# Kernel tuning notes

Measured on AMD Instinct MI355X. Metric: run time of the kernel, lower is better.

The kernel has to match this reference:

```python
import jax, jax.numpy as jnp
import numpy as np

FEAT_STRIDE = 16
SCALES = (8.0, 16.0, 32.0)
RATIOS = (0.5, 1.0, 2.0)
NEG_TH = 0.3
POS_TH = 0.7
FG_FRACTION = 0.5
RPN_BATCHSIZE = 256
A = 9  # num anchors per location


def generate_anchors(base_size=16, ratios=RATIOS, scales=SCALES):
    """Standard py-faster-rcnn anchor generation (ratio-major, scale-minor)."""
    base = np.array([0.0, 0.0, base_size - 1.0, base_size - 1.0])
    w = base[2] - base[0] + 1.0
    h = base[3] - base[1] + 1.0
    xc = base[0] + 0.5 * (w - 1.0)
    yc = base[1] + 0.5 * (h - 1.0)
    ratios = np.asarray(ratios, dtype=np.float64)
    scales = np.asarray(scales, dtype=np.float64)
    size = w * h
    ws = np.round(np.sqrt(size / ratios))          # [3]
    hs = np.round(ws * ratios)                     # [3]
    ws = (ws[:, None] * scales[None, :]).reshape(-1)  # [9]
    hs = (hs[:, None] * scales[None, :]).reshape(-1)
    anchors = np.stack([xc - 0.5 * (ws - 1.0), yc - 0.5 * (hs - 1.0),
                        xc + 0.5 * (ws - 1.0), yc + 0.5 * (hs - 1.0)], axis=1)
    return anchors.astype(np.float32)  # [9,4]


def _rank_desc(scores, mask):
    """Rank (0 = largest) of each element among masked entries, per row."""
    s = jnp.where(mask, scores, -jnp.inf)
    order = jnp.argsort(-s, axis=1)
    return jnp.argsort(order, axis=1)


def setup_inputs() -> dict:
    key = jax.random.key(0)
    k1, k2, k3, k4, k5, k6 = jax.random.split(key, 6)
    B, K, H, W = 32, 50, 64, 64
    IMG = float(H * FEAT_STRIDE)  # 1024
    rpn_cls_score = jax.random.normal(k1, (B, 2 * A, H, W), dtype=jnp.float32)
    x1 = jax.random.uniform(k2, (B, K)) * (IMG - 220.0)
    y1 = jax.random.uniform(k3, (B, K)) * (IMG - 220.0)
    bw = jax.random.uniform(k4, (B, K)) * 180.0 + 16.0
    bh = jax.random.uniform(k5, (B, K)) * 180.0 + 16.0
    gt_boxes = jnp.stack([x1, y1, x1 + bw, y1 + bh, jnp.ones((B, K))], axis=-1).astype(jnp.float32)
    im_info = jnp.tile(jnp.array([[IMG, IMG, 1.0]], dtype=jnp.float32), (B, 1))
    num_boxes = jax.random.randint(k6, (B,), 1, K + 1).astype(jnp.int32)
    return {"rpn_cls_score": rpn_cls_score, "gt_boxes": gt_boxes,
            "im_info": im_info, "num_boxes": num_boxes}


def reference(rpn_cls_score, gt_boxes, im_info, num_boxes):
    B = gt_boxes.shape[0]
    K = gt_boxes.shape[1]
    H, W = rpn_cls_score.shape[2], rpn_cls_score.shape[3]

    anchors = jnp.asarray(generate_anchors())  # [A,4]
    sx = jnp.arange(W, dtype=jnp.float32) * FEAT_STRIDE
    sy = jnp.arange(H, dtype=jnp.float32) * FEAT_STRIDE
    gx, gy = jnp.meshgrid(sx, sy)  # [H,W]
    shifts = jnp.stack([gx.ravel(), gy.ravel(), gx.ravel(), gy.ravel()], axis=1)  # [HW,4]
    all_anchors = (anchors[None, :, :] + shifts[:, None, :]).reshape(-1, 4)  # [N,4], N=HW*A
    N = all_anchors.shape[0]

    im_h, im_w = im_info[0, 0], im_info[0, 1]
    inside = ((all_anchors[:, 0] >= 0) & (all_anchors[:, 1] >= 0) &
              (all_anchors[:, 2] < im_w) & (all_anchors[:, 3] < im_h))  # [N]

    # pairwise IoU [B,N,K] with +1 pixel convention
    gt4 = gt_boxes[..., :4]
    ax1, ay1, ax2, ay2 = (all_anchors[None, :, None, i] for i in range(4))
    gx1, gy1, gx2, gy2 = (gt4[:, None, :, i] for i in range(4))
    iw = jnp.maximum(jnp.minimum(ax2, gx2) - jnp.maximum(ax1, gx1) + 1.0, 0.0)
    ih = jnp.maximum(jnp.minimum(ay2, gy2) - jnp.maximum(ay1, gy1) + 1.0, 0.0)
    inter = iw * ih
    a_area = ((all_anchors[:, 2] - all_anchors[:, 0] + 1.0) *
              (all_anchors[:, 3] - all_anchors[:, 1] + 1.0))[None, :, None]
    g_area = ((gt4[..., 2] - gt4[..., 0] + 1.0) * (gt4[..., 3] - gt4[..., 1] + 1.0))[:, None, :]
    ov = inter / (a_area + g_area - inter)
    valid = (jnp.arange(K)[None, :] < num_boxes[:, None])  # [B,K]
    ov = jnp.where(valid[:, None, :], ov, -1.0)

    max_ov = ov.max(axis=2)       # [B,N]
    argmax = ov.argmax(axis=2)    # [B,N]
    gt_max = ov.max(axis=1)       # [B,K]
    gt_max = jnp.where(gt_max == 0.0, 1e-5, gt_max)
    best = ((ov == gt_max[:, None, :]) & valid[:, None, :]).any(axis=2)  # [B,N]

    lab = jnp.full((B, N), -1.0, dtype=jnp.float32)
    lab = jnp.where(inside[None, :] & (max_ov < NEG_TH), 0.0, lab)
    lab = jnp.where(inside[None, :] & best, 1.0, lab)
    lab = jnp.where(inside[None, :] & (max_ov >= POS_TH), 1.0, lab)

    # random subsampling of positives / negatives
    skey = jax.random.key(42)
    kf, kb = jax.random.split(skey)
    num_fg = int(FG_FRACTION * RPN_BATCHSIZE)
    fg_mask = lab == 1.0
    rk_fg = _rank_desc(jax.random.uniform(kf, (B, N)), fg_mask)
    lab = jnp.where(fg_mask & (rk_fg >= num_fg), -1.0, lab)
    fg_cnt = (lab == 1.0).sum(axis=1)
    num_bg = RPN_BATCHSIZE - fg_cnt  # [B]
    bg_mask = lab == 0.0
    rk_bg = _rank_desc(jax.random.uniform(kb, (B, N)), bg_mask)
    lab = jnp.where(bg_mask & (rk_bg >= num_bg[:, None]), -1.0, lab)

    assigned = jnp.take_along_axis(gt4, argmax[:, :, None], axis=1)  # [B,N,4]
    ew = all_anchors[:, 2] - all_anchors[:, 0] + 1.0
    eh = all_anchors[:, 3] - all_anchors[:, 1] + 1.0
    ecx = all_anchors[:, 0] + 0.5 * ew
    ecy = all_anchors[:, 1] + 0.5 * eh
    gw = assigned[..., 2] - assigned[..., 0] + 1.0
    gh = assigned[..., 3] - assigned[..., 1] + 1.0
    gcx = assigned[..., 0] + 0.5 * gw
    gcy = assigned[..., 1] + 0.5 * gh
    tgt = jnp.stack([(gcx - ecx[None]) / ew[None], (gcy - ecy[None]) / eh[None],
                     jnp.log(gw / ew[None]), jnp.log(gh / eh[None])], axis=-1)  # [B,N,4]
    tgt = jnp.where(inside[None, :, None], tgt, 0.0)

    in_w = jnp.where((lab == 1.0)[:, :, None], 1.0, 0.0) * jnp.ones((4,), jnp.float32)
    num_examples = (lab >= 0.0).sum(axis=1).astype(jnp.float32)  # [B]
    out_w = jnp.where((lab >= 0.0)[:, :, None], (1.0 / num_examples)[:, None, None], 0.0) \
            * jnp.ones((4,), jnp.float32)

    labels_out = lab.reshape(B, H, W, A).transpose(0, 3, 1, 2).reshape(B, 1, A * H, W)
    tgt_out = tgt.reshape(B, H, W, A * 4).transpose(0, 3, 1, 2)
    in_w_out = in_w.reshape(B, H, W, A * 4).transpose(0, 3, 1, 2)
    out_w_out = out_w.reshape(B, H, W, A * 4).transpose(0, 3, 1, 2)
    return (labels_out, tgt_out, in_w_out, out_w_out)
```

## Files before the change

### kernel.cpp

```cpp
#include <hip/hip_runtime.h>
#include <stdint.h>

#pragma clang fp contract(off)

#define NBATCH 32
#define NK 50
#define NH 64
#define NW 64
#define NA 9
#define NN (NH * NW * NA)
#define BN (NBATCH * NN)
#define HWSZ (NH * NW)
#define BLK_PER_B (NN / 256)

constexpr size_t OFF_AMAX  = 0;
constexpr size_t OFF_PK    = OFF_AMAX + (size_t)BN * 4;
constexpr size_t OFF_GTMAX = OFF_PK + (size_t)BN * 4;
constexpr size_t OFF_NUMEX = OFF_GTMAX + (size_t)NBATCH * NK * 4;

constexpr size_t OUT_LAB  = 0;
constexpr size_t OUT_TGT  = (size_t)NBATCH * NA * HWSZ;
constexpr size_t OUT_INW  = OUT_TGT + (size_t)NBATCH * NA * 4 * HWSZ;
constexpr size_t OUT_OUTW = OUT_INW + (size_t)NBATCH * NA * 4 * HWSZ;

__constant__ float c_anch[NA][4] = {
    {-84.f, -40.f, 99.f, 55.f},    {-176.f, -88.f, 191.f, 103.f},
    {-360.f, -184.f, 375.f, 199.f}, {-56.f, -56.f, 71.f, 71.f},
    {-120.f, -120.f, 135.f, 135.f}, {-248.f, -248.f, 263.f, 263.f},
    {-36.f, -80.f, 51.f, 95.f},    {-80.f, -168.f, 95.f, 183.f},
    {-168.f, -344.f, 183.f, 359.f}};

struct TF2 { uint32_t a, b; };

__host__ __device__ constexpr uint32_t rotl32(uint32_t x, int d) {
  return (x << d) | (x >> (32 - d));
}

__host__ __device__ constexpr TF2 threefry2x32(uint32_t k0, uint32_t k1,
                                               uint32_t x0, uint32_t x1) {
  uint32_t ks2 = k0 ^ k1 ^ 0x1BD11BDAu;
  x0 += k0; x1 += k1;
  x0 += x1; x1 = rotl32(x1, 13); x1 ^= x0;
  x0 += x1; x1 = rotl32(x1, 15); x1 ^= x0;
  x0 += x1; x1 = rotl32(x1, 26); x1 ^= x0;
  x0 += x1; x1 = rotl32(x1, 6);  x1 ^= x0;
  x0 += k1; x1 += ks2 + 1u;
  x0 += x1; x1 = rotl32(x1, 17); x1 ^= x0;
  x0 += x1; x1 = rotl32(x1, 29); x1 ^= x0;
  x0 += x1; x1 = rotl32(x1, 16); x1 ^= x0;
  x0 += x1; x1 = rotl32(x1, 24); x1 ^= x0;
  x0 += ks2; x1 += k0 + 2u;
  x0 += x1; x1 = rotl32(x1, 13); x1 ^= x0;
  x0 += x1; x1 = rotl32(x1, 15); x1 ^= x0;
  x0 += x1; x1 = rotl32(x1, 26); x1 ^= x0;
  x0 += x1; x1 = rotl32(x1, 6);  x1 ^= x0;
  x0 += k0; x1 += k1 + 3u;
  x0 += x1; x1 = rotl32(x1, 17); x1 ^= x0;
  x0 += x1; x1 = rotl32(x1, 29); x1 ^= x0;
  x0 += x1; x1 = rotl32(x1, 16); x1 ^= x0;
  x0 += x1; x1 = rotl32(x1, 24); x1 ^= x0;
  x0 += k1; x1 += ks2 + 4u;
  x0 += x1; x1 = rotl32(x1, 13); x1 ^= x0;
  x0 += x1; x1 = rotl32(x1, 15); x1 ^= x0;
  x0 += x1; x1 = rotl32(x1, 26); x1 ^= x0;
  x0 += x1; x1 = rotl32(x1, 6);  x1 ^= x0;
  x0 += ks2; x1 += k0 + 5u;
  return TF2{x0, x1};
}

constexpr TF2 KEY_FG = threefry2x32(0u, 42u, 0u, 0u);
constexpr TF2 KEY_BG = threefry2x32(0u, 42u, 0u, 1u);

__device__ inline uint32_t rand23(uint32_t k0, uint32_t k1, uint32_t idx) {
  TF2 r = threefry2x32(k0, k1, 0u, idx);
  return (r.a ^ r.b) >> 9;
}

__device__ inline void anchor_of(int n, float& x1, float& y1, float& x2, float& y2) {
  int a = n % NA;
  int s = n / NA;
  int xx = s % NW;
  int yy = s / NW;
  float sx = (float)(xx * 16);
  float sy = (float)(yy * 16);
  x1 = c_anch[a][0] + sx; y1 = c_anch[a][1] + sy;
  x2 = c_anch[a][2] + sx; y2 = c_anch[a][3] + sy;
}

__device__ inline float iou1(float ax1, float ay1, float ax2, float ay2,
                             float gx1, float gy1, float gx2, float gy2) {
  float iw = fminf(ax2, gx2) - fmaxf(ax1, gx1) + 1.0f;
  iw = fmaxf(iw, 0.0f);
  float ih = fminf(ay2, gy2) - fmaxf(ay1, gy1) + 1.0f;
  ih = fmaxf(ih, 0.0f);
  float inter = iw * ih;
  float aa = (ax2 - ax1 + 1.0f) * (ay2 - ay1 + 1.0f);
  float ga = (gx2 - gx1 + 1.0f) * (gy2 - gy1 + 1.0f);
  return inter / (aa + ga - inter);
}

__global__ __launch_bounds__(256) void k_gtmax(const float* __restrict__ gt,
                                               const int* __restrict__ nbox,
                                               float* __restrict__ gtmax) {
  int b = blockIdx.x / NK;
  int k = blockIdx.x % NK;
  if (k >= nbox[b]) {
    if (threadIdx.x == 0) gtmax[blockIdx.x] = -1.0f;
    return;
  }
  const float* g = gt + ((size_t)b * NK + k) * 5;
  float gx1 = g[0], gy1 = g[1], gx2 = g[2], gy2 = g[3];
  float m = 0.0f;
#pragma unroll
  for (int a = 0; a < NA; ++a) {
    float bx1 = c_anch[a][0], by1 = c_anch[a][1];
    float bx2 = c_anch[a][2], by2 = c_anch[a][3];
    int ix_lo = max(0, (int)floorf((gx1 - 1.0f - bx2) * 0.0625f) - 1);
    int ix_hi = min(NW - 1, (int)ceilf((gx2 + 1.0f - bx1) * 0.0625f) + 1);
    int iy_lo = max(0, (int)floorf((gy1 - 1.0f - by2) * 0.0625f) - 1);
    int iy_hi = min(NH - 1, (int)ceilf((gy2 + 1.0f - by1) * 0.0625f) + 1);
    if (ix_lo > ix_hi || iy_lo > iy_hi) continue;
    int nx = ix_hi - ix_lo + 1;
    int ny = iy_hi - iy_lo + 1;
    int lg = 32 - __clz(nx - 1);
    int tot = ny << lg;
    unsigned mask = (1u << lg) - 1u;
    for (int c = threadIdx.x; c < tot; c += 256) {
      int ixo = c & mask;
      if (ixo >= nx) continue;
      int ix = ix_lo + ixo;
      int iy = iy_lo + (c >> lg);
      float sx = (float)(ix * 16), sy = (float)(iy * 16);
      m = fmaxf(m, iou1(bx1 + sx, by1 + sy, bx2 + sx, by2 + sy, gx1, gy1, gx2, gy2));
    }
  }
  for (int o = 1; o < 64; o <<= 1) m = fmaxf(m, __shfl_xor(m, o));
  __shared__ float ws4[4];
  if ((threadIdx.x & 63) == 0) ws4[threadIdx.x >> 6] = m;
  __syncthreads();
  if (threadIdx.x == 0) {
    m = fmaxf(fmaxf(ws4[0], ws4[1]), fmaxf(ws4[2], ws4[3]));
    if (m == 0.0f) m = 1e-5f;
    gtmax[blockIdx.x] = m;
  }
}

__global__ __launch_bounds__(256) void k_label(const float* __restrict__ gt,
                                               const int* __restrict__ nbox,
                                               const float* __restrict__ gtmax,
                                               const float* __restrict__ iminfo,
                                               unsigned* __restrict__ pkarr,
                                               int* __restrict__ amax) {
  int b = blockIdx.x / BLK_PER_B;
  int n = (blockIdx.x % BLK_PER_B) * 256 + threadIdx.x;
  __shared__ float sg[NK * 5];
  __shared__ float sgm[NK];
  __shared__ float sga[NK];
  if (threadIdx.x < NK * 5) sg[threadIdx.x] = gt[(size_t)b * NK * 5 + threadIdx.x];
  if (threadIdx.x < NK) sgm[threadIdx.x] = gtmax[b * NK + threadIdx.x];
  __syncthreads();
  if (threadIdx.x < NK) {
    float* gg = sg + threadIdx.x * 5;
    sga[threadIdx.x] = (gg[2] - gg[0] + 1.0f) * (gg[3] - gg[1] + 1.0f);
  }
  __syncthreads();

  float ax1, ay1, ax2, ay2;
  anchor_of(n, ax1, ay1, ax2, ay2);
  float aa = (ax2 - ax1 + 1.0f) * (ay2 - ay1 + 1.0f);
  int m = nbox[b];
  float best = -2.0f;
  int bi = 0;
  bool isbest = false;
  for (int k = 0; k < m; ++k) {
    float iw = fminf(ax2, sg[k * 5 + 2]) - fmaxf(ax1, sg[k * 5]) + 1.0f;
    iw = fmaxf(iw, 0.0f);
    float ih = fminf(ay2, sg[k * 5 + 3]) - fmaxf(ay1, sg[k * 5 + 1]) + 1.0f;
    ih = fmaxf(ih, 0.0f);
    float inter = iw * ih;
    float ov = inter / (aa + sga[k] - inter);
    if (ov > best) { best = ov; bi = k; }
    if (ov == sgm[k]) isbest = true;
  }
  float imh = iminfo[0], imw = iminfo[1];
  bool inside = (ax1 >= 0.0f) && (ay1 >= 0.0f) && (ax2 < imw) && (ay2 < imh);
  int lab = -1;
  if (inside) {
    if (best < 0.3f) lab = 0;
    if (isbest) lab = 1;
    if (best >= 0.7f) lab = 1;
  }
  int t = b * NN + n;
  uint32_t kk0 = (lab == 1) ? KEY_FG.a : KEY_BG.a;
  uint32_t kk1 = (lab == 1) ? KEY_FG.b : KEY_BG.b;
  uint32_t v = rand23(kk0, kk1, (uint32_t)t);
  pkarr[t] = (v << 2) | (uint32_t)(lab + 1);
  amax[t] = bi;
}

__global__ __launch_bounds__(1024) void k_select(unsigned* __restrict__ pkarr,
                                                 float* __restrict__ numex) {
  int b = blockIdx.x >> 1;
  int cls = blockIdx.x & 1;
  int base_lab = b * NN;
  unsigned wantcode = (cls == 0) ? 2u : 1u;
  int tid = threadIdx.x;

  __shared__ unsigned h1s[4096];
  __shared__ unsigned listV[2048];
  __shared__ unsigned listI[2048];
  __shared__ unsigned waveTot[4];
  __shared__ int sFG, sBG, sBs, sR1, sCross;
  __shared__ unsigned sCnt;
  for (int i = tid; i < 4096; i += 1024) h1s[i] = 0;
  if (tid == 0) { sFG = 0; sBG = 0; sCross = -1; sCnt = 0; }
  __syncthreads();

  const uint4* pk4 = (const uint4*)(pkarr + base_lab);

  int cfg = 0, cbg = 0;
  for (int i = tid; i < NN / 4; i += 1024) {
    uint4 P4 = pk4[i];
    unsigned pks[4] = {P4.x, P4.y, P4.z, P4.w};
#pragma unroll
    for (int j = 0; j < 4; ++j) {
      unsigned code = pks[j] & 3u;
      cfg += (code == 2u);
      cbg += (code == 1u);
      if (code == wantcode) atomicAdd(&h1s[pks[j] >> 13], 1u);
    }
  }
  for (int o = 1; o < 64; o <<= 1) { cfg += __shfl_xor(cfg, o); cbg += __shfl_xor(cbg, o); }
  if ((tid & 63) == 0) { atomicAdd(&sFG, cfg); atomicAdd(&sBG, cbg); }
  __syncthreads();

  int fg = sFG, bg = sBG;
  int fgk = min(fg, 128);
  int total, C;
  if (cls == 0) {
    total = fg; C = 128;
  } else {
    total = bg; C = 256 - fgk;
    if (tid == 0) numex[b] = (float)(fgk + min(bg, C));
  }
  if (total <= C) return;

  unsigned myChunk = 0, suf = 0;
  if (tid < 256) {
    for (int j = 0; j < 16; ++j) myChunk += h1s[tid * 16 + j];
    unsigned ss = myChunk;
    int lane = tid & 63;
#pragma unroll
    for (int o = 1; o < 64; o <<= 1) {
      unsigned t2 = __shfl_down(ss, o);
      if (lane + o < 64) ss += t2;
    }
    suf = ss;
    if (lane == 0) waveTot[tid >> 6] = ss;
  }
  __syncthreads();
  if (tid < 256) {
    int w = tid >> 6;
    for (int w2 = w + 1; w2 < 4; ++w2) suf += waveTot[w2];
    if (suf >= (unsigned)C) atomicMax(&sCross, tid);
  }
  __syncthreads();
  if (tid == sCross) {
    unsigned cum = suf - myChunk;
    int i = tid * 16 + 15;
    for (;; --i) {
      unsigned c = h1s[i];
      if (cum + c >= (unsigned)C) break;
      cum += c;
    }
    sBs = i; sR1 = (int)((unsigned)C - cum);
  }
  __syncthreads();
  int Bs = sBs;
  unsigned r1 = (unsigned)sR1;

  for (int i = tid; i < NN / 4; i += 1024) {
    uint4 P4 = pk4[i];
    unsigned pks[4] = {P4.x, P4.y, P4.z, P4.w};
#pragma unroll
    for (int j = 0; j < 4; ++j) {
      if ((pks[j] & 3u) == wantcode) {
        unsigned v = pks[j] >> 2;
        int bk = (int)(v >> 11);
        int n = 4 * i + j;
        if (bk < Bs) {
          pkarr[base_lab + n] = pks[j] & ~3u;
        } else if (bk == Bs) {
          unsigned p = atomicAdd(&sCnt, 1u);
          if (p < 2048u) { listV[p] = v; listI[p] = (unsigned)n; }
        }
      }
    }
  }
  __syncthreads();

  unsigned L = min(sCnt, 2048u);
  for (unsigned i = tid; i < L; i += 1024) {
    unsigned vi = listV[i], xi = listI[i];
    unsigned rank = 0;
    for (unsigned j = 0; j < L; ++j) {
      unsigned vj = listV[j], xj = listI[j];
      rank += (vj > vi) || (vj == vi && xj < xi);
    }
    if (rank >= r1) pkarr[base_lab + (int)xi] = vi << 2;
  }
}

__global__ __launch_bounds__(256) void k_out(const float* __restrict__ gt,
                                             const unsigned* __restrict__ pkarr,
                                             const int* __restrict__ amax,
                                             const float* __restrict__ iminfo,
                                             const float* __restrict__ numex,
                                             float* __restrict__ out) {
  int q = blockIdx.x * 256 + threadIdx.x;
  if (q >= (int)(OUT_TGT / 4)) return;
  int xx4 = q & 15;
  int yy = (q >> 4) & 63;
  int ba = q >> 10;
  int a = ba % NA;
  int b = ba / NA;
  int xx0 = xx4 * 4;
  int yx0 = yy * NW + xx0;

  float imh = iminfo[0], imw = iminfo[1];
  float inv_ne = 1.0f / numex[b];

  float labf[4], iwv[4], owv[4], tg[4][4];
#pragma unroll
  for (int u = 0; u < 4; ++u) {
    int xx = xx0 + u;
    int n = (yy * NW + xx) * NA + a;
    int bn = b * NN + n;
    int lab = (int)(pkarr[bn] & 3u) - 1;
    labf[u] = (float)lab;
    float ax1, ay1, ax2, ay2;
    anchor_of(n, ax1, ay1, ax2, ay2);
    bool inside = (ax1 >= 0.0f) && (ay1 >= 0.0f) && (ax2 < imw) && (ay2 < imh);
    float t0 = 0.f, t1 = 0.f, t2 = 0.f, t3 = 0.f;
    if (inside) {
      const float* g = gt + ((size_t)b * NK + amax[bn]) * 5;
      float ew = ax2 - ax1 + 1.0f, eh = ay2 - ay1 + 1.0f;
      float ecx = ax1 + 0.5f * ew, ecy = ay1 + 0.5f * eh;
      float gw = g[2] - g[0] + 1.0f, gh = g[3] - g[1] + 1.0f;
      float gcx = g[0] + 0.5f * gw, gcy = g[1] + 0.5f * gh;
      t0 = (gcx - ecx) / ew;
      t1 = (gcy - ecy) / eh;
      t2 = logf(gw / ew);
      t3 = logf(gh / eh);
    }
    tg[0][u] = t0; tg[1][u] = t1; tg[2][u] = t2; tg[3][u] = t3;
    iwv[u] = (lab == 1) ? 1.0f : 0.0f;
    owv[u] = (lab >= 0) ? inv_ne : 0.0f;
  }

  *(float4*)(out + OUT_LAB + (size_t)ba * HWSZ + yx0) =
      make_float4(labf[0], labf[1], labf[2], labf[3]);
  size_t tb = OUT_TGT + ((size_t)b * NA * 4 + a * 4) * HWSZ + yx0;
#pragma unroll
  for (int d = 0; d < 4; ++d)
    *(float4*)(out + tb + (size_t)d * HWSZ) =
        make_float4(tg[d][0], tg[d][1], tg[d][2], tg[d][3]);
  size_t ib = OUT_INW + ((size_t)b * NA * 4 + a * 4) * HWSZ + yx0;
  float4 iw4 = make_float4(iwv[0], iwv[1], iwv[2], iwv[3]);
#pragma unroll
  for (int d = 0; d < 4; ++d) *(float4*)(out + ib + (size_t)d * HWSZ) = iw4;
  size_t ob = OUT_OUTW + ((size_t)b * NA * 4 + a * 4) * HWSZ + yx0;
  float4 ow4 = make_float4(owv[0], owv[1], owv[2], owv[3]);
#pragma unroll
  for (int d = 0; d < 4; ++d) *(float4*)(out + ob + (size_t)d * HWSZ) = ow4;
}

extern "C" void kernel_launch(void* const* d_in, const int* in_sizes, int n_in,
                              void* d_out, int out_size, void* d_ws, size_t ws_size,
                              hipStream_t stream) {
  (void)in_sizes; (void)n_in; (void)out_size; (void)ws_size;
  const float* gt     = (const float*)d_in[1];
  const float* iminfo = (const float*)d_in[2];
  const int*   nbox   = (const int*)d_in[3];
  float* out = (float*)d_out;
  char* ws = (char*)d_ws;

  int*      amax  = (int*)(ws + OFF_AMAX);
  unsigned* pkarr = (unsigned*)(ws + OFF_PK);
  float*    gtmax = (float*)(ws + OFF_GTMAX);
  float*    numex = (float*)(ws + OFF_NUMEX);

  k_gtmax<<<NBATCH * NK, 256, 0, stream>>>(gt, nbox, gtmax);
  k_label<<<BN / 256, 256, 0, stream>>>(gt, nbox, gtmax, iminfo, pkarr, amax);
  k_select<<<2 * NBATCH, 1024, 0, stream>>>(pkarr, numex);
  k_out<<<(int)(OUT_TGT / 4 / 256), 256, 0, stream>>>(gt, pkarr, amax, iminfo, numex, out);
}
```

Baseline: 162.7 us.

## Replace per-element subsampling writes with per-batch threshold applied in output kernel

The select kernel now handles foreground and background in one block per batch. It builds both histograms in a single pass and, instead of rewriting disabled labels back into the packed array, computes a (value, index) cutoff for each class. The output kernel then applies that cutoff while reading labels, which removes the scattered global writes and the second class pass over the array. The cost is half as many select blocks (32), so the histogram pass has less parallelism, plus a small extra comparison in the output kernel. Boundary buckets are now capped at 1024 entries instead of 2048, which could overflow on adversarial inputs.

```diff
diff --git a/kernel.cpp b/kernel.cpp
--- a/kernel.cpp
+++ b/kernel.cpp
@@ -17,6 +17,7 @@
 constexpr size_t OFF_PK    = OFF_AMAX + (size_t)BN * 4;
 constexpr size_t OFF_GTMAX = OFF_PK + (size_t)BN * 4;
 constexpr size_t OFF_NUMEX = OFF_GTMAX + (size_t)NBATCH * NK * 4;
+constexpr size_t OFF_THR   = OFF_NUMEX + (size_t)NBATCH * 4;
 
 constexpr size_t OUT_LAB  = 0;
 constexpr size_t OUT_TGT  = (size_t)NBATCH * NA * HWSZ;
@@ -198,22 +199,23 @@
   amax[t] = bi;
 }
 
-__global__ __launch_bounds__(1024) void k_select(unsigned* __restrict__ pkarr,
-                                                 float* __restrict__ numex) {
-  int b = blockIdx.x >> 1;
-  int cls = blockIdx.x & 1;
+__global__ __launch_bounds__(1024) void k_select(const unsigned* __restrict__ pkarr,
+                                                 float* __restrict__ numex,
+                                                 uint4* __restrict__ thr) {
+  int b = blockIdx.x;
   int base_lab = b * NN;
-  unsigned wantcode = (cls == 0) ? 2u : 1u;
   int tid = threadIdx.x;
 
-  __shared__ unsigned h1s[4096];
-  __shared__ unsigned listV[2048];
-  __shared__ unsigned listI[2048];
+  __shared__ unsigned hF[4096];
+  __shared__ unsigned hB[4096];
+  __shared__ unsigned listV[2][1024];
+  __shared__ unsigned listI[2][1024];
   __shared__ unsigned waveTot[4];
-  __shared__ int sFG, sBG, sBs, sR1, sCross;
-  __shared__ unsigned sCnt;
-  for (int i = tid; i < 4096; i += 1024) h1s[i] = 0;
-  if (tid == 0) { sFG = 0; sBG = 0; sCross = -1; sCnt = 0; }
+  __shared__ int sFG, sBG, sCross, sBs[2], sR1[2];
+  __shared__ unsigned sCnt[2];
+  __shared__ unsigned sV[2], sI[2];
+  for (int i = tid; i < 4096; i += 1024) { hF[i] = 0; hB[i] = 0; }
+  if (tid == 0) { sFG = 0; sBG = 0; sCnt[0] = 0; sCnt[1] = 0; }
   __syncthreads();
 
   const uint4* pk4 = (const uint4*)(pkarr + base_lab);
@@ -227,7 +229,8 @@
       unsigned code = pks[j] & 3u;
       cfg += (code == 2u);
       cbg += (code == 1u);
-      if (code == wantcode) atomicAdd(&h1s[pks[j] >> 13], 1u);
+      if (code == 2u) atomicAdd(&hF[pks[j] >> 13], 1u);
+      else if (code == 1u) atomicAdd(&hB[pks[j] >> 13], 1u);
     }
   }
   for (int o = 1; o < 64; o <<= 1) { cfg += __shfl_xor(cfg, o); cbg += __shfl_xor(cbg, o); }
@@ -236,78 +239,97 @@
 
   int fg = sFG, bg = sBG;
   int fgk = min(fg, 128);
-  int total, C;
-  if (cls == 0) {
-    total = fg; C = 128;
-  } else {
-    total = bg; C = 256 - fgk;
-    if (tid == 0) numex[b] = (float)(fgk + min(bg, C));
-  }
-  if (total <= C) return;
-
-  unsigned myChunk = 0, suf = 0;
-  if (tid < 256) {
-    for (int j = 0; j < 16; ++j) myChunk += h1s[tid * 16 + j];
-    unsigned ss = myChunk;
-    int lane = tid & 63;
-#pragma unroll
-    for (int o = 1; o < 64; o <<= 1) {
-      unsigned t2 = __shfl_down(ss, o);
-      if (lane + o < 64) ss += t2;
-    }
-    suf = ss;
-    if (lane == 0) waveTot[tid >> 6] = ss;
-  }
-  __syncthreads();
-  if (tid < 256) {
-    int w = tid >> 6;
-    for (int w2 = w + 1; w2 < 4; ++w2) suf += waveTot[w2];
-    if (suf >= (unsigned)C) atomicMax(&sCross, tid);
-  }
-  __syncthreads();
-  if (tid == sCross) {
-    unsigned cum = suf - myChunk;
-    int i = tid * 16 + 15;
-    for (;; --i) {
-      unsigned c = h1s[i];
-      if (cum + c >= (unsigned)C) break;
-      cum += c;
-    }
-    sBs = i; sR1 = (int)((unsigned)C - cum);
-  }
-  __syncthreads();
-  int Bs = sBs;
-  unsigned r1 = (unsigned)sR1;
-
+  int Cf = 128;
+  int Cb = 256 - fgk;
+  if (tid == 0) numex[b] = (float)(fgk + min(bg, Cb));
+  bool actF = fg > Cf;
+  bool actB = bg > Cb;
+  if (!actF && !actB) {
+    if (tid == 0) *(&thr[b]) = make_uint4(0u, 0x7FFFFFFFu, 0u, 0x7FFFFFFFu);
+    return;
+  }
+
+  for (int cls = 0; cls < 2; ++cls) {
+    bool act = (cls == 0) ? actF : actB;
+    if (!act) continue;
+    const unsigned* h = (cls == 0) ? hF : hB;
+    unsigned C = (unsigned)((cls == 0) ? Cf : Cb);
+    if (tid == 0) sCross = -1;
+    __syncthreads();
+    unsigned myChunk = 0, suf = 0;
+    if (tid < 256) {
+      for (int j = 0; j < 16; ++j) myChunk += h[tid * 16 + j];
+      unsigned ss = myChunk;
+      int lane = tid & 63;
+#pragma unroll
+      for (int o = 1; o < 64; o <<= 1) {
+        unsigned t2 = __shfl_down(ss, o);
+        if (lane + o < 64) ss += t2;
+      }
+      suf = ss;
+      if (lane == 0) waveTot[tid >> 6] = ss;
+    }
+    __syncthreads();
+    if (tid < 256) {
+      int w = tid >> 6;
+      for (int w2 = w + 1; w2 < 4; ++w2) suf += waveTot[w2];
+      if (suf >= C) atomicMax(&sCross, tid);
+    }
+    __syncthreads();
+    if (tid == sCross) {
+      unsigned cum = suf - myChunk;
+      int i = tid * 16 + 15;
+      for (;; --i) {
+        unsigned c = h[i];
+        if (cum + c >= C) break;
+        cum += c;
+      }
+      sBs[cls] = i; sR1[cls] = (int)(C - cum);
+    }
+    __syncthreads();
+  }
+
+  int BsF = actF ? sBs[0] : -1;
+  int BsB = actB ? sBs[1] : -1;
   for (int i = tid; i < NN / 4; i += 1024) {
     uint4 P4 = pk4[i];
     unsigned pks[4] = {P4.x, P4.y, P4.z, P4.w};
 #pragma unroll
     for (int j = 0; j < 4; ++j) {
-      if ((pks[j] & 3u) == wantcode) {
-        unsigned v = pks[j] >> 2;
-        int bk = (int)(v >> 11);
-        int n = 4 * i + j;
-        if (bk < Bs) {
-          pkarr[base_lab + n] = pks[j] & ~3u;
-        } else if (bk == Bs) {
-          unsigned p = atomicAdd(&sCnt, 1u);
-          if (p < 2048u) { listV[p] = v; listI[p] = (unsigned)n; }
-        }
+      unsigned code = pks[j] & 3u;
+      int bk = (int)(pks[j] >> 13);
+      int cls = -1;
+      if (code == 2u && bk == BsF) cls = 0;
+      else if (code == 1u && bk == BsB) cls = 1;
+      if (cls >= 0) {
+        unsigned p = atomicAdd(&sCnt[cls], 1u);
+        if (p < 1024u) { listV[cls][p] = pks[j] >> 2; listI[cls][p] = (unsigned)(4 * i + j); }
       }
     }
   }
   __syncthreads();
 
-  unsigned L = min(sCnt, 2048u);
-  for (unsigned i = tid; i < L; i += 1024) {
-    unsigned vi = listV[i], xi = listI[i];
-    unsigned rank = 0;
-    for (unsigned j = 0; j < L; ++j) {
-      unsigned vj = listV[j], xj = listI[j];
-      rank += (vj > vi) || (vj == vi && xj < xi);
-    }
-    if (rank >= r1) pkarr[base_lab + (int)xi] = vi << 2;
+  for (int cls = 0; cls < 2; ++cls) {
+    bool act = (cls == 0) ? actF : actB;
+    if (!act) continue;
+    unsigned L = min(sCnt[cls], 1024u);
+    unsigned target = (unsigned)(sR1[cls] - 1);
+    for (unsigned i = tid; i < L; i += 1024) {
+      unsigned vi = listV[cls][i], xi = listI[cls][i];
+      unsigned rank = 0;
+      for (unsigned j = 0; j < L; ++j) {
+        unsigned vj = listV[cls][j], xj = listI[cls][j];
+        rank += (vj > vi) || (vj == vi && xj < xi);
+      }
+      if (rank == target) { sV[cls] = vi; sI[cls] = xi; }
+    }
+  }
+  __syncthreads();
+  if (tid == 0) {
+    uint4 t;
+    t.x = actF ? sV[0] : 0u;  t.y = actF ? sI[0] : 0x7FFFFFFFu;
+    t.z = actB ? sV[1] : 0u;  t.w = actB ? sI[1] : 0x7FFFFFFFu;
+    thr[b] = t;
   }
 }
 
@@ -316,6 +338,7 @@
                                              const int* __restrict__ amax,
                                              const float* __restrict__ iminfo,
                                              const float* __restrict__ numex,
+                                             const uint4* __restrict__ thr,
                                              float* __restrict__ out) {
   int q = blockIdx.x * 256 + threadIdx.x;
   if (q >= (int)(OUT_TGT / 4)) return;
@@ -329,6 +352,7 @@
 
   float imh = iminfo[0], imw = iminfo[1];
   float inv_ne = 1.0f / numex[b];
+  uint4 th = thr[b];
 
   float labf[4], iwv[4], owv[4], tg[4][4];
 #pragma unroll
@@ -336,7 +360,15 @@
     int xx = xx0 + u;
     int n = (yy * NW + xx) * NA + a;
     int bn = b * NN + n;
-    int lab = (int)(pkarr[bn] & 3u) - 1;
+    unsigned pk = pkarr[bn];
+    int lab = (int)(pk & 3u) - 1;
+    if (lab >= 0) {
+      unsigned v = pk >> 2;
+      unsigned vs = (lab == 1) ? th.x : th.z;
+      unsigned is = (lab == 1) ? th.y : th.w;
+      bool keep = (v > vs) || (v == vs && (unsigned)n <= is);
+      if (!keep) lab = -1;
+    }
     labf[u] = (float)lab;
     float ax1, ay1, ax2, ay2;
     anchor_of(n, ax1, ay1, ax2, ay2);
@@ -389,9 +421,10 @@
   unsigned* pkarr = (unsigned*)(ws + OFF_PK);
   float*    gtmax = (float*)(ws + OFF_GTMAX);
   float*    numex = (float*)(ws + OFF_NUMEX);
+  uint4*    thr   = (uint4*)(ws + OFF_THR);
 
   k_gtmax<<<NBATCH * NK, 256, 0, stream>>>(gt, nbox, gtmax);
   k_label<<<BN / 256, 256, 0, stream>>>(gt, nbox, gtmax, iminfo, pkarr, amax);
-  k_select<<<2 * NBATCH, 1024, 0, stream>>>(pkarr, numex);
-  k_out<<<(int)(OUT_TGT / 4 / 256), 256, 0, stream>>>(gt, pkarr, amax, iminfo, numex, out);
-}
+  k_select<<<NBATCH, 1024, 0, stream>>>(pkarr, numex, thr);
+  k_out<<<(int)(OUT_TGT / 4 / 256), 256, 0, stream>>>(gt, pkarr, amax, iminfo, numex, thr, out);
+}
```

New measurement: 162.8 us. About the same (+0.1%).
